# Optimization experiments

Measured on AMD Instinct MI355X. Metric: run time of the kernel, lower is better.

## Reference

```python
import jax, jax.numpy as jnp
import numpy as np

B, T, C, H, W = 1, 8, 64, 96, 96
DG = 16  # deform groups
MAX_RES = 5.0  # max_residue_magnitude


def lrelu(x):
    return jnp.where(x >= 0, x, 0.1 * x)


def conv(x, w, b):
    y = jax.lax.conv_general_dilated(x, w, (1, 1), 'SAME',
                                     dimension_numbers=('NCHW', 'OIHW', 'NCHW'))
    return y + b[None, :, None, None]


def mod_deform_conv2d(x, offset, mask, weight, bias, dg):
    # Modulated deformable conv v2: 3x3 kernel, stride 1, pad 1, dil 1.
    Bs, Cin, Hs, Ws = x.shape
    K = 9
    cpg = Cin // dg
    Cout = weight.shape[0]
    off = offset.reshape(Bs, dg, K, 2, Hs, Ws)  # (y, x) per tap
    m = mask.reshape(Bs, dg, K, Hs, Ws)
    ky = jnp.repeat(jnp.arange(3), 3).astype(x.dtype)
    kx = jnp.tile(jnp.arange(3), 3).astype(x.dtype)
    # base sampling positions: out_pos - pad + tap*dil
    py = (jnp.arange(Hs, dtype=x.dtype) - 1.0)[None, :, None] + ky[:, None, None]  # (K,H,1)
    px = (jnp.arange(Ws, dtype=x.dtype) - 1.0)[None, None, :] + kx[:, None, None]  # (K,1,W)
    sy = off[:, :, :, 0] + py  # (B,dg,K,H,W)
    sx = off[:, :, :, 1] + px
    y0 = jnp.floor(sy)
    x0 = jnp.floor(sx)
    fy = sy - y0
    fx = sx - x0
    y0i = y0.astype(jnp.int32)
    x0i = x0.astype(jnp.int32)
    xf = x.reshape(Bs, dg, cpg, Hs * Ws)

    def gather(yi, xi, wgt):
        valid = (yi >= 0) & (yi < Hs) & (xi >= 0) & (xi < Ws)
        idx = (jnp.clip(yi, 0, Hs - 1) * Ws + jnp.clip(xi, 0, Ws - 1))
        idx = idx.reshape(Bs, dg, 1, K * Hs * Ws)
        v = jnp.take_along_axis(xf, idx, axis=3).reshape(Bs, dg, cpg, K, Hs, Ws)
        return v * (wgt * valid)[:, :, None]

    val = (gather(y0i, x0i, (1 - fy) * (1 - fx))
           + gather(y0i, x0i + 1, (1 - fy) * fx)
           + gather(y0i + 1, x0i, fy * (1 - fx))
           + gather(y0i + 1, x0i + 1, fy * fx))
    cols = val * m[:, :, None]  # (B,dg,cpg,K,H,W)
    wr = weight.reshape(Cout, dg, cpg, K)
    out = jnp.einsum('ogck,bgckhw->bohw', wr, cols)
    return out + bias[None, :, None, None]


def deform_align(xin, cond, p):
    h = lrelu(conv(cond, p['ow1'], p['ob1']))
    h = lrelu(conv(h, p['ow2'], p['ob2']))
    h = lrelu(conv(h, p['ow3'], p['ob3']))
    out = conv(h, p['ow4'], p['ob4'])
    offset = MAX_RES * jnp.tanh(out[:, :18 * DG])
    mask = jax.nn.sigmoid(out[:, 18 * DG:])
    return mod_deform_conv2d(xin, offset, mask, p['dw'], p['db'], DG)


def bidir_prop(x, params):
    t = x.shape[1]
    spatial = [x[:, i] for i in range(t)]
    feats = {}
    for name, rev in (('backward_', True), ('forward_', False)):
        p = params[name]
        order = list(range(t))[::-1] if rev else list(range(t))
        out_list = []
        prop = jnp.zeros_like(spatial[0])
        for i, idx in enumerate(order):
            cur = spatial[idx]
            if i > 0:
                feat_n2 = out_list[-2] if i > 1 else jnp.zeros_like(prop)
                cond = jnp.concatenate([prop, cur, feat_n2], axis=1)
                prop = deform_align(jnp.concatenate([prop, feat_n2], axis=1), cond, p)
            if name == 'forward_':
                feat = jnp.concatenate([cur, feats['backward_'][idx], prop], axis=1)
            else:
                feat = jnp.concatenate([cur, prop], axis=1)
            prop = prop + conv(lrelu(conv(feat, p['bw1'], p['bb1'])), p['bw2'], p['bb2'])
            out_list.append(prop)
        feats[name] = out_list[::-1] if rev else out_list
    fw, fb = params['fusion']
    outs = [conv(jnp.concatenate([feats['backward_'][i], feats['forward_'][i]], axis=1), fw, fb)
            for i in range(t)]
    return jnp.stack(outs, axis=1) + x


def setup_inputs() -> dict:
    key = jax.random.key(0)
    ks = iter(jax.random.split(key, 64))

    def w(*shape):
        return jax.random.normal(next(ks), shape, jnp.float32) * 0.03

    def b(n):
        return jnp.zeros((n,), jnp.float32)

    d = {'x': jax.random.normal(next(ks), (B, T, C, H, W), jnp.float32)}
    for pre, bb1_in in (('b', 2 * C), ('f', 3 * C)):
        d[pre + '_dw'] = w(C, 2 * C, 3, 3); d[pre + '_db'] = b(C)
        d[pre + '_ow1'] = w(C, 3 * C, 3, 3); d[pre + '_ob1'] = b(C)
        d[pre + '_ow2'] = w(C, C, 3, 3); d[pre + '_ob2'] = b(C)
        d[pre + '_ow3'] = w(C, C, 3, 3); d[pre + '_ob3'] = b(C)
        d[pre + '_ow4'] = w(27 * DG, C, 3, 3); d[pre + '_ob4'] = b(27 * DG)
        d[pre + '_bw1'] = w(C, bb1_in, 3, 3); d[pre + '_bb1'] = b(C)
        d[pre + '_bw2'] = w(C, C, 3, 3); d[pre + '_bb2'] = b(C)
    d['fus_w'] = w(C, 2 * C, 1, 1)
    d['fus_b'] = b(C)
    return d


def _assemble(b_dw, b_db, b_ow1, b_ob1, b_ow2, b_ob2, b_ow3, b_ob3, b_ow4, b_ob4,
              b_bw1, b_bb1, b_bw2, b_bb2,
              f_dw, f_db, f_ow1, f_ob1, f_ow2, f_ob2, f_ow3, f_ob3, f_ow4, f_ob4,
              f_bw1, f_bb1, f_bw2, f_bb2, fus_w, fus_b):
    return {
        'backward_': dict(dw=b_dw, db=b_db, ow1=b_ow1, ob1=b_ob1, ow2=b_ow2, ob2=b_ob2,
                          ow3=b_ow3, ob3=b_ob3, ow4=b_ow4, ob4=b_ob4,
                          bw1=b_bw1, bb1=b_bb1, bw2=b_bw2, bb2=b_bb2),
        'forward_': dict(dw=f_dw, db=f_db, ow1=f_ow1, ob1=f_ob1, ow2=f_ow2, ob2=f_ob2,
                         ow3=f_ow3, ob3=f_ob3, ow4=f_ow4, ob4=f_ob4,
                         bw1=f_bw1, bb1=f_bb1, bw2=f_bw2, bb2=f_bb2),
        'fusion': (fus_w, fus_b),
    }


def reference(x, b_dw, b_db, b_ow1, b_ob1, b_ow2, b_ob2, b_ow3, b_ob3, b_ow4, b_ob4,
              b_bw1, b_bb1, b_bw2, b_bb2,
              f_dw, f_db, f_ow1, f_ob1, f_ow2, f_ob2, f_ow3, f_ob3, f_ow4, f_ob4,
              f_bw1, f_bb1, f_bw2, f_bb2, fus_w, fus_b):
    params = _assemble(b_dw, b_db, b_ow1, b_ob1, b_ow2, b_ob2, b_ow3, b_ob3, b_ow4, b_ob4,
                       b_bw1, b_bb1, b_bw2, b_bb2,
                       f_dw, f_db, f_ow1, f_ob1, f_ow2, f_ob2, f_ow3, f_ob3, f_ow4, f_ob4,
                       f_bw1, f_bb1, f_bw2, f_bb2, fus_w, fus_b)
    return bidir_prop(x, params)
```

## Files before the change

### kernel.cpp

```cpp
#include <hip/hip_runtime.h>
#include <cstddef>
#include <cstdint>

#define HW96 9216
#define FRAME (64 * 9216)

typedef unsigned short ushort_t;
typedef __attribute__((ext_vector_type(8))) short bf16x8;
typedef __attribute__((ext_vector_type(4))) float f32x4;
typedef __attribute__((ext_vector_type(4))) unsigned u32x4;
typedef __attribute__((ext_vector_type(8))) ushort_t u16x8;
typedef __attribute__((ext_vector_type(4))) ushort_t u16x4;

__device__ __forceinline__ float unpk(unsigned p) {
    return __uint_as_float(p & 0xFFFF0000u) + __uint_as_float(p << 16);
}
__device__ __forceinline__ unsigned pk(float v) {
    unsigned u = __float_as_uint(v);
    unsigned hi = u & 0xFFFF0000u;
    float rem = v - __uint_as_float(hi);
    unsigned r = __float_as_uint(rem);
    unsigned lo = (r + 0x7FFFu + ((r >> 16) & 1u)) >> 16;
    return hi | (lo & 0xFFFFu);
}
__device__ __forceinline__ void split16(float v, ushort_t& h, ushort_t& l) {
    unsigned u = __float_as_uint(v);
    h = (ushort_t)(u >> 16);
    float rem = v - __uint_as_float(u & 0xFFFF0000u);
    unsigned r = __float_as_uint(rem);
    l = (ushort_t)((r + 0x7FFFu + ((r >> 16) & 1u)) >> 16);
}
__device__ __forceinline__ ushort_t bf16rnd(float v) {
    unsigned u = __float_as_uint(v);
    return (ushort_t)((u + 0x7FFFu + ((u >> 16) & 1u)) >> 16);
}
__device__ __forceinline__ float bfh(ushort_t h) {
    return __uint_as_float(((unsigned)h) << 16);
}

struct FragJob { const float* src; ushort_t* dst; int O, I, OT, KC, mode; };
struct FragJobs { FragJob j[15]; };

__global__ __launch_bounds__(256) void frag_all_k(FragJobs jobs) {
    const FragJob& J = jobs.j[blockIdx.y];
    int idx = blockIdx.x * 256 + threadIdx.x;
    int total = ((J.mode == 0) ? 9 : 1) * J.KC * J.OT * 512;
    if (idx >= total) return;
    int jj = idx & 7;
    int lane = (idx >> 3) & 63;
    int rem = idx >> 9;
    int ot = rem % J.OT;
    rem /= J.OT;
    int cc = rem % J.KC;
    int t = rem / J.KC;
    int o = ot * 16 + (lane & 15);
    float wv = 0.f;
    if (J.mode == 0) {
        int ci = cc * 32 + (lane >> 4) * 8 + jj;
        if (o < J.O && ci < J.I) wv = J.src[(o * J.I + ci) * 9 + t];
    } else if (J.mode == 1) {
        int K = cc * 32 + (lane >> 4) * 8 + jj;
        int g = K / 72, r2 = K % 72;
        int tap = r2 >> 3, c = r2 & 7;
        int ci = g * 8 + c;
        if (o < J.O && ci < J.I) wv = J.src[(o * J.I + ci) * 9 + tap];
    } else {
        int ci = cc * 32 + (lane >> 4) * 8 + jj;
        if (o < J.O && ci < J.I) wv = J.src[o * J.I + ci];
    }
    ushort_t h, l;
    split16(wv, h, l);
    J.dst[idx] = h;
    J.dst[total + idx] = l;
}

__global__ __launch_bounds__(256) void pack_tr_k(const float* __restrict__ src,
                                                 unsigned* __restrict__ dst,
                                                 ushort_t* __restrict__ dsth) {
    const int t = blockIdx.y;
    const int px0 = blockIdx.x * 64;
    __shared__ unsigned tile[64 * 65];
    const float* s = src + (size_t)t * FRAME;
    unsigned* d = dst + (size_t)t * FRAME;
    ushort_t* dh = dsth + (size_t)t * FRAME;
#pragma unroll
    for (int it = 0; it < 16; ++it) {
        int e = it * 256 + threadIdx.x;
        int p = e & 63, ch = e >> 6;
        tile[ch * 65 + p] = pk(s[(size_t)ch * HW96 + px0 + p]);
    }
    __syncthreads();
#pragma unroll
    for (int it = 0; it < 16; ++it) {
        int e = it * 256 + threadIdx.x;
        int ch = e & 63, p = e >> 6;
        unsigned v = tile[ch * 65 + p];
        d[(size_t)(px0 + p) * 64 + ch] = v;
        dh[(size_t)(px0 + p) * 64 + ch] = (ushort_t)(v >> 16);
    }
}

template <int TERMS>
__global__ __launch_bounds__(128, 3) void convm_k(
    const unsigned* __restrict__ s0, const unsigned* __restrict__ s1,
    const unsigned* __restrict__ s2, int b0, int b1, int b2, int nsrc,
    const ushort_t* __restrict__ wfrag, int KCfull,
    const float* __restrict__ bias, const float* __restrict__ addsrc,
    const float* __restrict__ addsrc2, const float* __restrict__ abias,
    ushort_t* __restrict__ outhi, unsigned* __restrict__ outpk, int act) {
    const int tid = threadIdx.x;
    const int lane = tid & 63;
    const int w = tid >> 6;
    const int h = blockIdx.x & 1;
    const int bseg = blockIdx.x >> 1;
    const int ot = h * 2 + w;
    const int xb = (bseg % 6) * 16;
    const int y = bseg / 6;
    const int n = lane & 15;
    const int quad = lane >> 4;

    __shared__ __align__(16) ushort_t ldsH[3 * 18 * 72];
    __shared__ __align__(16) ushort_t ldsL[3 * 18 * 72];

    int jst[4], jok[4], joff[4], jbase[4];
#pragma unroll
    for (int i = 0; i < 4; ++i) {
        int e = tid + i * 128;
        int rc = e >> 3, cg = e & 7;
        int r = rc / 18, col = rc - r * 18;
        int gy = y - 1 + r, gx = xb - 1 + col;
        jst[i] = (e < 432);
        jok[i] = jst[i] && ((unsigned)gy < 96u) && ((unsigned)gx < 96u);
        joff[i] = (gy * 96 + gx) * 64 + cg * 8;
        jbase[i] = rc * 72 + cg * 8;
    }

    f32x4 acc0, acc1;
#pragma unroll
    for (int r = 0; r < 4; ++r) { acc0[r] = 0.f; acc1[r] = 0.f; }

    const size_t hlOff = (size_t)9 * KCfull * 4 * 512;

    for (int j = 0; j < nsrc; ++j) {
        const unsigned* sv = (j == 0) ? s0 : (j == 1 ? s1 : s2);
        const int base = (j == 0) ? b0 : (j == 1 ? b1 : b2);
        __syncthreads();
#pragma unroll
        for (int i = 0; i < 4; ++i) {
            if (jst[i]) {
                u32x4 a, b;
                if (jok[i]) {
                    a = *(const u32x4*)(sv + joff[i]);
                    b = *(const u32x4*)(sv + joff[i] + 4);
                } else {
#pragma unroll
                    for (int q = 0; q < 4; ++q) { a[q] = 0; b[q] = 0; }
                }
                u32x4 H, L;
#pragma unroll
                for (int q = 0; q < 2; ++q) {
                    H[q] = (a[2 * q] >> 16) | (a[2 * q + 1] & 0xFFFF0000u);
                    L[q] = (a[2 * q] & 0xFFFFu) | (a[2 * q + 1] << 16);
                    H[2 + q] = (b[2 * q] >> 16) | (b[2 * q + 1] & 0xFFFF0000u);
                    L[2 + q] = (b[2 * q] & 0xFFFFu) | (b[2 * q + 1] << 16);
                }
                *(u32x4*)(ldsH + jbase[i]) = H;
                *(u32x4*)(ldsL + jbase[i]) = L;
            }
        }
        __syncthreads();
        bf16x8 pAh[5], pAl[5], pBh[5], pBl[5];
#pragma unroll
        for (int s = 0; s < 23; ++s) {
            if (s >= 5) {
                const int u = s - 5;
                const bf16x8 Ah = pAh[u % 5];
                const bf16x8 Bh = pBh[u % 5], Bl = pBl[u % 5];
                if (u & 1) {
                    acc1 = __builtin_amdgcn_mfma_f32_16x16x32_bf16(Ah, Bh, acc1, 0, 0, 0);
                    if (TERMS == 3)
                        acc1 = __builtin_amdgcn_mfma_f32_16x16x32_bf16(pAl[u % 5], Bh, acc1, 0, 0, 0);
                    acc1 = __builtin_amdgcn_mfma_f32_16x16x32_bf16(Ah, Bl, acc1, 0, 0, 0);
                } else {
                    acc0 = __builtin_amdgcn_mfma_f32_16x16x32_bf16(Ah, Bh, acc0, 0, 0, 0);
                    if (TERMS == 3)
                        acc0 = __builtin_amdgcn_mfma_f32_16x16x32_bf16(pAl[u % 5], Bh, acc0, 0, 0, 0);
                    acc0 = __builtin_amdgcn_mfma_f32_16x16x32_bf16(Ah, Bl, acc0, 0, 0, 0);
                }
            }
            if (s < 18) {
                const int t = s >> 1, cc2 = s & 1;
                const int ky = t / 3, kx = t % 3;
                const int ccor = base + cc2;
                const ushort_t* ab =
                    wfrag + (((size_t)(t * KCfull + ccor) * 4 + ot) * 64 + lane) * 8;
                pAh[s % 5] = *(const bf16x8*)ab;
                if (TERMS == 3) pAl[s % 5] = *(const bf16x8*)(ab + hlOff);
                const int lb = (ky * 18 + n + kx) * 72 + cc2 * 32 + quad * 8;
                pBh[s % 5] = *(const bf16x8*)(ldsH + lb);
                pBl[s % 5] = *(const bf16x8*)(ldsL + lb);
            }
        }
    }

    const int px = y * 96 + xb + n;
    u16x4 hi4;
#pragma unroll
    for (int r = 0; r < 4; ++r) {
        int cout = ot * 16 + quad * 4 + r;
        float v = acc0[r] + acc1[r] + bias[cout];
        if (act) v = (v >= 0.f) ? v : 0.1f * v;
        if (addsrc) {
            size_t off = (size_t)cout * HW96 + px;
            v += addsrc[off] + addsrc2[off] + abias[cout];
        }
        outpk[(size_t)px * 64 + cout] = pk(v);
        hi4[r] = bf16rnd(v);
    }
    if (outhi)
        *(u16x4*)(outhi + (size_t)px * 64 + ot * 16 + quad * 4) = hi4;
}

__global__ __launch_bounds__(128, 3) void convh_k(
    const ushort_t* __restrict__ s0, const ushort_t* __restrict__ s1,
    const ushort_t* __restrict__ s2, int b0, int b1, int b2, int nsrc,
    const ushort_t* __restrict__ wfrag, int KCfull,
    const float* __restrict__ bias, ushort_t* __restrict__ outhi, int act) {
    const int tid = threadIdx.x;
    const int lane = tid & 63;
    const int w = tid >> 6;
    const int h = blockIdx.x & 1;
    const int bseg = blockIdx.x >> 1;
    const int ot = h * 2 + w;
    const int xb = (bseg % 6) * 16;
    const int y = bseg / 6;
    const int n = lane & 15;
    const int quad = lane >> 4;

    __shared__ __align__(16) ushort_t ldsH[3 * 18 * 72];

    int jst[4], jok[4], joff[4], jbase[4];
#pragma unroll
    for (int i = 0; i < 4; ++i) {
        int e = tid + i * 128;
        int rc = e >> 3, cg = e & 7;
        int r = rc / 18, col = rc - r * 18;
        int gy = y - 1 + r, gx = xb - 1 + col;
        jst[i] = (e < 432);
        jok[i] = jst[i] && ((unsigned)gy < 96u) && ((unsigned)gx < 96u);
        joff[i] = (gy * 96 + gx) * 64 + cg * 8;
        jbase[i] = rc * 72 + cg * 8;
    }

    f32x4 acc0, acc1;
#pragma unroll
    for (int r = 0; r < 4; ++r) { acc0[r] = 0.f; acc1[r] = 0.f; }

    for (int j = 0; j < nsrc; ++j) {
        const ushort_t* sv = (j == 0) ? s0 : (j == 1 ? s1 : s2);
        const int base = (j == 0) ? b0 : (j == 1 ? b1 : b2);
        __syncthreads();
#pragma unroll
        for (int i = 0; i < 4; ++i) {
            if (jst[i]) {
                u16x8 a;
                if (jok[i]) {
                    a = *(const u16x8*)(sv + joff[i]);
                } else {
#pragma unroll
                    for (int q = 0; q < 8; ++q) a[q] = 0;
                }
                *(u16x8*)(ldsH + jbase[i]) = a;
            }
        }
        __syncthreads();
        bf16x8 pAh[5], pBh[5];
#pragma unroll
        for (int s = 0; s < 23; ++s) {
            if (s >= 5) {
                const int u = s - 5;
                const bf16x8 Ah = pAh[u % 5];
                const bf16x8 Bh = pBh[u % 5];
                if (u & 1)
                    acc1 = __builtin_amdgcn_mfma_f32_16x16x32_bf16(Ah, Bh, acc1, 0, 0, 0);
                else
                    acc0 = __builtin_amdgcn_mfma_f32_16x16x32_bf16(Ah, Bh, acc0, 0, 0, 0);
            }
            if (s < 18) {
                const int t = s >> 1, cc2 = s & 1;
                const int ky = t / 3, kx = t % 3;
                const int ccor = base + cc2;
                const ushort_t* ab =
                    wfrag + (((size_t)(t * KCfull + ccor) * 4 + ot) * 64 + lane) * 8;
                pAh[s % 5] = *(const bf16x8*)ab;
                const int lb = (ky * 18 + n + kx) * 72 + cc2 * 32 + quad * 8;
                pBh[s % 5] = *(const bf16x8*)(ldsH + lb);
            }
        }
    }

    const int px = y * 96 + xb + n;
    u16x4 hi4;
#pragma unroll
    for (int r = 0; r < 4; ++r) {
        int cout = ot * 16 + quad * 4 + r;
        float v = acc0[r] + acc1[r] + bias[cout];
        if (act) v = (v >= 0.f) ? v : 0.1f * v;
        hi4[r] = bf16rnd(v);
    }
    *(u16x4*)(outhi + (size_t)px * 64 + ot * 16 + quad * 4) = hi4;
}

__global__ __launch_bounds__(256) void dconv_fused_k(
    const ushort_t* __restrict__ sAh, const ushort_t* __restrict__ sBh,
    const ushort_t* __restrict__ hAh, const ushort_t* __restrict__ w4,
    const float* __restrict__ ob4, const ushort_t* __restrict__ dwf,
    int ngr4, float* __restrict__ pacc) {
    const int tid = threadIdx.x;
    const int lane = tid & 63;
    const int w = tid >> 6;
    const int h = blockIdx.x & 1;
    const int seg = blockIdx.x >> 1;
    const int xb = (seg % 6) * 16;
    const int y = seg / 6;
    const int n = lane & 15;
    const int quad = lane >> 4;

    __shared__ __align__(16) char smem[15232 + 18944];
    float* rawS = (float*)smem;
    ushort_t* ldsAH = (ushort_t*)(smem + 15232);
    ushort_t* colsH = (ushort_t*)(smem + 15232);
    ushort_t* colsL = colsH + 4736;

    const int nrounds = ngr4 >> 1;
    const int ng = nrounds * 4;
    const int g0 = h * ng;
    const int otO_s = (g0 * 18) >> 4;
    const int otO_e = (g0 * 18 + ng * 18 - 1) >> 4;
    const int nO = otO_e - otO_s + 1;
    const int otM_s = (288 + g0 * 9) >> 4;
    const int otM_e = (288 + g0 * 9 + ng * 9 - 1) >> 4;
    const int nM = otM_e - otM_s + 1;
    const int nt = nO + nM;
    const int rowOffO = otO_s * 16;
    const int rowOffM = otM_s * 16 - nO * 16;

#pragma unroll
    for (int i = 0; i < 2; ++i) {
        int e = tid + i * 256;
        if (e < 432) {
            int rc = e >> 3, cg = e & 7;
            int r = rc / 18, col = rc - r * 18;
            int gy = y - 1 + r, gx = xb - 1 + col;
            bool ok = ((unsigned)gy < 96u) && ((unsigned)gx < 96u);
            u16x8 a;
            if (ok) {
                a = *(const u16x8*)(hAh + (gy * 96 + gx) * 64 + cg * 8);
            } else {
#pragma unroll
                for (int q = 0; q < 8; ++q) a[q] = 0;
            }
            *(u16x8*)(ldsAH + rc * 72 + cg * 8) = a;
        }
    }
    __syncthreads();

#pragma unroll 1
    for (int j = 0; j < 4; ++j) {
        const int idx = j * 4 + w;
        if (idx >= nt) break;
        const int ot = (idx < nO) ? (otO_s + idx) : (otM_s + (idx - nO));
        f32x4 a0, a1;
#pragma unroll
        for (int r = 0; r < 4; ++r) { a0[r] = 0.f; a1[r] = 0.f; }
        bf16x8 pAh[5], pBh[5];
#pragma unroll
        for (int s = 0; s < 23; ++s) {
            if (s >= 5) {
                const int u = s - 5;
                const bf16x8 Ah = pAh[u % 5];
                const bf16x8 Bh = pBh[u % 5];
                if (u & 1)
                    a1 = __builtin_amdgcn_mfma_f32_16x16x32_bf16(Ah, Bh, a1, 0, 0, 0);
                else
                    a0 = __builtin_amdgcn_mfma_f32_16x16x32_bf16(Ah, Bh, a0, 0, 0, 0);
            }
            if (s < 18) {
                const int t = s >> 1, cc2 = s & 1;
                const int ky = t / 3, kx = t % 3;
                const ushort_t* ab =
                    w4 + (((size_t)s * 28 + ot) * 64 + lane) * 8;
                pAh[s % 5] = *(const bf16x8*)ab;
                const int lb = (ky * 18 + n + kx) * 72 + cc2 * 32 + quad * 8;
                pBh[s % 5] = *(const bf16x8*)(ldsAH + lb);
            }
        }
#pragma unroll
        for (int r = 0; r < 4; ++r) {
            int cout = ot * 16 + quad * 4 + r;
            float v = a0[r] + a1[r] + (cout < 432 ? ob4[cout] : 0.f);
            rawS[(idx * 16 + quad * 4 + r) * 17 + n] = v;
        }
    }

    f32x4 acc0, acc1;
#pragma unroll
    for (int r = 0; r < 4; ++r) { acc0[r] = 0.f; acc1[r] = 0.f; }

    for (int gci = 0; gci < nrounds; ++gci) {
        const int gc = h * nrounds + gci;
        __syncthreads();
#pragma unroll
        for (int i = 0; i < 3; ++i) {
            int e = tid + i * 256;
            if (e < 576) {
                int p = e & 15;
                int r = e >> 4;
                int gl = r / 9, k = r - gl * 9;
                int g = gc * 4 + gl;
                float ry = rawS[(g * 18 + k * 2 + 0 - rowOffO) * 17 + p];
                float rx = rawS[(g * 18 + k * 2 + 1 - rowOffO) * 17 + p];
                float rm = rawS[(288 + g * 9 + k - rowOffM) * 17 + p];
                float oy = 5.f * (1.f - 2.f / (1.f + __expf(2.f * ry)));
                float ox = 5.f * (1.f - 2.f / (1.f + __expf(2.f * rx)));
                float m = 1.f / (1.f + __expf(-rm));
                float sy = oy + (float)(y - 1 + k / 3);
                float sx = ox + (float)(xb + p - 1 + k % 3);
                float fy0 = floorf(sy), fx0 = floorf(sx);
                float fy = sy - fy0, fx = sx - fx0;
                int y0 = (int)fy0, x0 = (int)fx0;
                int y1 = y0 + 1, x1 = x0 + 1;
                bool vy0 = (unsigned)y0 < 96u, vy1 = (unsigned)y1 < 96u;
                bool vx0 = (unsigned)x0 < 96u, vx1 = (unsigned)x1 < 96u;
                int cy0 = min(max(y0, 0), 95), cy1 = min(max(y1, 0), 95);
                int cx0 = min(max(x0, 0), 95), cx1 = min(max(x1, 0), 95);
                float w00 = (1.f - fy) * (1.f - fx) * ((vy0 && vx0) ? 1.f : 0.f);
                float w01 = (1.f - fy) * fx * ((vy0 && vx1) ? 1.f : 0.f);
                float w10 = fy * (1.f - fx) * ((vy1 && vx0) ? 1.f : 0.f);
                float w11 = fy * fx * ((vy1 && vx1) ? 1.f : 0.f);
                const ushort_t* src = (g < 8) ? sAh : sBh;
                int cb = (g & 7) * 8;
                int kbase = p * 296 + gl * 72 + k * 8;
                ushort_t hh[8], ll[8];
                if (src) {
                    u16x8 c00 = *(const u16x8*)(src + (cy0 * 96 + cx0) * 64 + cb);
                    u16x8 c01 = *(const u16x8*)(src + (cy0 * 96 + cx1) * 64 + cb);
                    u16x8 c10 = *(const u16x8*)(src + (cy1 * 96 + cx0) * 64 + cb);
                    u16x8 c11 = *(const u16x8*)(src + (cy1 * 96 + cx1) * 64 + cb);
#pragma unroll
                    for (int c = 0; c < 8; ++c) {
                        float v = w00 * bfh(c00[c]) + w01 * bfh(c01[c]) +
                                  w10 * bfh(c10[c]) + w11 * bfh(c11[c]);
                        split16(v * m, hh[c], ll[c]);
                    }
                } else {
#pragma unroll
                    for (int c = 0; c < 8; ++c) { hh[c] = 0; ll[c] = 0; }
                }
                u32x4 H, L;
#pragma unroll
                for (int q = 0; q < 4; ++q) {
                    H[q] = (unsigned)hh[2 * q] | ((unsigned)hh[2 * q + 1] << 16);
                    L[q] = (unsigned)ll[2 * q] | ((unsigned)ll[2 * q + 1] << 16);
                }
                *(u32x4*)(colsH + kbase) = H;
                *(u32x4*)(colsL + kbase) = L;
            }
        }
        __syncthreads();
        bf16x8 qAh[4], qBh[4], qBl[4];
#pragma unroll
        for (int s = 0; s < 13; ++s) {
            if (s >= 4) {
                const int u = s - 4;
                const bf16x8 Ah = qAh[u % 4];
                const bf16x8 Bh = qBh[u % 4], Bl = qBl[u % 4];
                if (u & 1) {
                    acc1 = __builtin_amdgcn_mfma_f32_16x16x32_bf16(Ah, Bh, acc1, 0, 0, 0);
                    acc1 = __builtin_amdgcn_mfma_f32_16x16x32_bf16(Ah, Bl, acc1, 0, 0, 0);
                } else {
                    acc0 = __builtin_amdgcn_mfma_f32_16x16x32_bf16(Ah, Bh, acc0, 0, 0, 0);
                    acc0 = __builtin_amdgcn_mfma_f32_16x16x32_bf16(Ah, Bl, acc0, 0, 0, 0);
                }
            }
            if (s < 9) {
                const int cc = gc * 9 + s;
                const ushort_t* ab = dwf + (((size_t)cc * 4 + w) * 64 + lane) * 8;
                qAh[s % 4] = *(const bf16x8*)ab;
                const int lb = n * 296 + s * 32 + quad * 8;
                qBh[s % 4] = *(const bf16x8*)(colsH + lb);
                qBl[s % 4] = *(const bf16x8*)(colsL + lb);
            }
        }
    }

    const int pidx = y * 96 + xb + n;
#pragma unroll
    for (int r = 0; r < 4; ++r) {
        int cout = w * 16 + quad * 4 + r;
        pacc[(size_t)h * FRAME + (size_t)cout * HW96 + pidx] =
            acc0[r] + acc1[r];
    }
}

__global__ __launch_bounds__(256) void dcomb_k(const float* __restrict__ pacc,
                                               const float* __restrict__ dbias,
                                               unsigned* __restrict__ outpk) {
    const int px0 = blockIdx.x * 64;
    __shared__ unsigned tile[64 * 65];
#pragma unroll
    for (int it = 0; it < 16; ++it) {
        int e = it * 256 + threadIdx.x;
        int p = e & 63, ch = e >> 6;
        size_t off = (size_t)ch * HW96 + px0 + p;
        float v = pacc[off] + pacc[(size_t)FRAME + off] + dbias[ch];
        tile[ch * 65 + p] = pk(v);
    }
    __syncthreads();
#pragma unroll
    for (int it = 0; it < 16; ++it) {
        int e = it * 256 + threadIdx.x;
        int ch = e & 63, p = e >> 6;
        outpk[(size_t)(px0 + p) * 64 + ch] = tile[ch * 65 + p];
    }
}

__global__ __launch_bounds__(128) void fusem_k(
    const unsigned* __restrict__ featB, const unsigned* __restrict__ featF,
    const float* __restrict__ x, const ushort_t* __restrict__ wfrag,
    const float* __restrict__ bias, float* __restrict__ out) {
    const int tid = threadIdx.x;
    const int lane = tid & 63;
    const int w = tid >> 6;
    const int h = blockIdx.x & 1;
    const int bseg = blockIdx.x >> 1;
    const int t = blockIdx.y;
    const int ot = h * 2 + w;
    const int xb = (bseg % 6) * 16;
    const int y = bseg / 6;
    const int n = lane & 15;
    const int quad = lane >> 4;

    __shared__ __align__(16) ushort_t ldsH[16 * 144];
    __shared__ __align__(16) ushort_t ldsL[16 * 144];

    const int p = tid >> 3, cg = tid & 7;
    const int off = ((y * 96 + xb + p) * 64 + cg * 8);
#pragma unroll
    for (int i = 0; i < 2; ++i) {
        const unsigned* sv =
            (i == 0 ? featB : featF) + (size_t)t * FRAME;
        u32x4 a = *(const u32x4*)(sv + off);
        u32x4 b = *(const u32x4*)(sv + off + 4);
        u32x4 H, L;
#pragma unroll
        for (int q = 0; q < 2; ++q) {
            H[q] = (a[2 * q] >> 16) | (a[2 * q + 1] & 0xFFFF0000u);
            L[q] = (a[2 * q] & 0xFFFFu) | (a[2 * q + 1] << 16);
            H[2 + q] = (b[2 * q] >> 16) | (b[2 * q + 1] & 0xFFFF0000u);
            L[2 + q] = (b[2 * q] & 0xFFFFu) | (b[2 * q + 1] << 16);
        }
        *(u32x4*)(ldsH + p * 144 + i * 64 + cg * 8) = H;
        *(u32x4*)(ldsL + p * 144 + i * 64 + cg * 8) = L;
    }
    __syncthreads();

    f32x4 acc0, acc1;
#pragma unroll
    for (int r = 0; r < 4; ++r) { acc0[r] = 0.f; acc1[r] = 0.f; }
    const size_t hlOff = (size_t)4 * 4 * 512;
#pragma unroll
    for (int cc = 0; cc < 4; ++cc) {
        const ushort_t* ab = wfrag + (((size_t)cc * 4 + ot) * 64 + lane) * 8;
        bf16x8 Ah = *(const bf16x8*)ab;
        bf16x8 Al = *(const bf16x8*)(ab + hlOff);
        int lb = n * 144 + cc * 32 + quad * 8;
        bf16x8 Bh = *(const bf16x8*)(ldsH + lb);
        bf16x8 Bl = *(const bf16x8*)(ldsL + lb);
        if (cc & 1) {
            acc1 = __builtin_amdgcn_mfma_f32_16x16x32_bf16(Ah, Bh, acc1, 0, 0, 0);
            acc1 = __builtin_amdgcn_mfma_f32_16x16x32_bf16(Al, Bh, acc1, 0, 0, 0);
            acc1 = __builtin_amdgcn_mfma_f32_16x16x32_bf16(Ah, Bl, acc1, 0, 0, 0);
        } else {
            acc0 = __builtin_amdgcn_mfma_f32_16x16x32_bf16(Ah, Bh, acc0, 0, 0, 0);
            acc0 = __builtin_amdgcn_mfma_f32_16x16x32_bf16(Al, Bh, acc0, 0, 0, 0);
            acc0 = __builtin_amdgcn_mfma_f32_16x16x32_bf16(Ah, Bl, acc0, 0, 0, 0);
        }
    }

    const int pidx = y * 96 + xb + n;
    const float* xt = x + (size_t)t * FRAME;
    float* od = out + (size_t)t * FRAME;
#pragma unroll
    for (int r = 0; r < 4; ++r) {
        int cout = ot * 16 + quad * 4 + r;
        size_t o2 = (size_t)cout * HW96 + pidx;
        od[o2] = acc0[r] + acc1[r] + bias[cout] + xt[o2];
    }
}

extern "C" void kernel_launch(void* const* d_in, const int* in_sizes, int n_in,
                              void* d_out, int out_size, void* d_ws,
                              size_t ws_size, hipStream_t stream) {
    const float* x = (const float*)d_in[0];
    auto gp = [&](int i) { return (const float*)d_in[i]; };

    struct DirP {
        const float *dw, *db, *ow1, *ob1, *ow2, *ob2, *ow3, *ob3, *ow4, *ob4,
            *bw1, *bb1, *bw2, *bb2;
    };
    DirP Pb{gp(1), gp(2), gp(3), gp(4), gp(5), gp(6), gp(7),
            gp(8), gp(9), gp(10), gp(11), gp(12), gp(13), gp(14)};
    DirP Pf{gp(15), gp(16), gp(17), gp(18), gp(19), gp(20), gp(21),
            gp(22), gp(23), gp(24), gp(25), gp(26), gp(27), gp(28)};
    const float* fus_w = gp(29);
    const float* fus_b = gp(30);

    unsigned* featBpk = (unsigned*)d_ws;
    unsigned* featFpk = featBpk + (size_t)8 * FRAME;
    unsigned* xpk = featFpk + (size_t)8 * FRAME;
    unsigned* Dpk = xpk + (size_t)8 * FRAME;
    unsigned* hApk = Dpk + FRAME;
    unsigned* hBpk = hApk + FRAME;
    ushort_t* fragp = (ushort_t*)(hBpk + FRAME);

    auto falloc = [&](size_t nelem) {
        ushort_t* p = fragp;
        fragp += nelem;
        return p;
    };

    struct DirW { ushort_t *ow1, *ow2, *ow3, *ow4, *bw1, *bw2, *dw; int bw1KC; };
    FragJobs fj;
    int nf = 0;
    auto fjob = [&](const float* src, int O, int I, int OT, int KC) {
        ushort_t* dst = falloc((size_t)2 * 9 * KC * OT * 512);
        fj.j[nf++] = FragJob{src, dst, O, I, OT, KC, 0};
        return dst;
    };
    auto fjobd = [&](const float* src) {
        ushort_t* dst = falloc((size_t)2 * 36 * 4 * 512);
        fj.j[nf++] = FragJob{src, dst, 64, 128, 4, 36, 1};
        return dst;
    };
    DirW Wb, Wf;
    Wb.ow1 = fjob(Pb.ow1, 64, 192, 4, 6);
    Wb.ow2 = fjob(Pb.ow2, 64, 64, 4, 2);
    Wb.ow3 = fjob(Pb.ow3, 64, 64, 4, 2);
    Wb.ow4 = fjob(Pb.ow4, 432, 64, 28, 2);
    Wb.bw1 = fjob(Pb.bw1, 64, 128, 4, 4);
    Wb.bw1KC = 4;
    Wb.bw2 = fjob(Pb.bw2, 64, 64, 4, 2);
    Wb.dw = fjobd(Pb.dw);
    Wf.ow1 = fjob(Pf.ow1, 64, 192, 4, 6);
    Wf.ow2 = fjob(Pf.ow2, 64, 64, 4, 2);
    Wf.ow3 = fjob(Pf.ow3, 64, 64, 4, 2);
    Wf.ow4 = fjob(Pf.ow4, 432, 64, 28, 2);
    Wf.bw1 = fjob(Pf.bw1, 64, 192, 4, 6);
    Wf.bw1KC = 6;
    Wf.bw2 = fjob(Pf.bw2, 64, 64, 4, 2);
    Wf.dw = fjobd(Pf.dw);
    ushort_t* Wfus = falloc((size_t)2 * 4 * 4 * 512);
    fj.j[nf++] = FragJob{fus_w, Wfus, 64, 128, 4, 4, 2};
    frag_all_k<<<dim3(1008, 15), 256, 0, stream>>>(fj);

    float* pacc = (float*)((((uintptr_t)fragp) + 15) & ~(uintptr_t)15);
    ushort_t* featBh = (ushort_t*)(pacc + (size_t)2 * FRAME);
    ushort_t* featFh = featBh + (size_t)8 * FRAME;
    ushort_t* xh = featFh + (size_t)8 * FRAME;
    ushort_t* hAh = (ushort_t*)hApk;
    ushort_t* hBh = (ushort_t*)hBpk;

    pack_tr_k<<<dim3(144, 8), 256, 0, stream>>>(x, xpk, xh);

    auto convm = [&](const unsigned* a, const unsigned* b, const unsigned* c2,
                     const ushort_t* frag, int KCfull, const float* bias,
                     const float* add, const float* add2, const float* abias,
                     ushort_t* outhi, unsigned* out, int act, int terms) {
        const unsigned* srcs[3] = {a, b, c2};
        const unsigned* S[3] = {nullptr, nullptr, nullptr};
        int B[3] = {0, 0, 0};
        int ns = 0;
        for (int j = 0; j < 3; ++j)
            if (srcs[j]) {
                S[ns] = srcs[j];
                B[ns] = j * 2;
                ++ns;
            }
        if (terms == 2)
            convm_k<2><<<1152, 128, 0, stream>>>(S[0], S[1], S[2], B[0], B[1],
                                                 B[2], ns, frag, KCfull, bias,
                                                 add, add2, abias, outhi, out,
                                                 act);
        else
            convm_k<3><<<1152, 128, 0, stream>>>(S[0], S[1], S[2], B[0], B[1],
                                                 B[2], ns, frag, KCfull, bias,
                                                 add, add2, abias, outhi, out,
                                                 act);
    };

    auto convh = [&](const ushort_t* a, const ushort_t* b, const ushort_t* c2,
                     const ushort_t* frag, int KCfull, const float* bias,
                     ushort_t* out, int act) {
        const ushort_t* srcs[3] = {a, b, c2};
        const ushort_t* S[3] = {nullptr, nullptr, nullptr};
        int B[3] = {0, 0, 0};
        int ns = 0;
        for (int j = 0; j < 3; ++j)
            if (srcs[j]) {
                S[ns] = srcs[j];
                B[ns] = j * 2;
                ++ns;
            }
        convh_k<<<1152, 128, 0, stream>>>(S[0], S[1], S[2], B[0], B[1], B[2],
                                          ns, frag, KCfull, bias, out, act);
    };

    for (int dir = 0; dir < 2; ++dir) {
        const DirP& P = dir ? Pf : Pb;
        const DirW& W = dir ? Wf : Wb;
        unsigned* feat = dir ? featFpk : featBpk;
        ushort_t* feath = dir ? featFh : featBh;
        const unsigned* prev1 = nullptr;
        const unsigned* prev2 = nullptr;
        const ushort_t* prev1h = nullptr;
        const ushort_t* prev2h = nullptr;
        for (int i = 0; i < 8; ++i) {
            int idx = dir ? i : 7 - i;
            const unsigned* cur = xpk + (size_t)idx * FRAME;
            const ushort_t* curh = xh + (size_t)idx * FRAME;
            bool hasD = false;
            if (i > 0) {
                convh(prev1h, curh, prev2h, W.ow1, 6, P.ob1, hAh, 1);
                convh(hAh, nullptr, nullptr, W.ow2, 2, P.ob2, hBh, 1);
                convh(hBh, nullptr, nullptr, W.ow3, 2, P.ob3, hAh, 1);
                int ngr4 = (prev2 != nullptr) ? 4 : 2;
                dconv_fused_k<<<1152, 256, 0, stream>>>(
                    prev1h, prev2h, hAh, W.ow4, P.ob4, W.dw, ngr4, pacc);
                dcomb_k<<<144, 256, 0, stream>>>(pacc, P.db, Dpk);
                hasD = true;
            }
            unsigned* dst = feat + (size_t)idx * FRAME;
            ushort_t* dsth = feath + (size_t)idx * FRAME;
            if (dir == 0) {
                convm(cur, hasD ? Dpk : nullptr, nullptr, W.bw1, W.bw1KC,
                      P.bb1, nullptr, nullptr, nullptr, nullptr, hBpk, 1, 2);
            } else {
                convm(cur, featBpk + (size_t)idx * FRAME,
                      hasD ? Dpk : nullptr, W.bw1, W.bw1KC, P.bb1, nullptr,
                      nullptr, nullptr, nullptr, hBpk, 1, 2);
            }
            convm(hBpk, nullptr, nullptr, W.bw2, 2, P.bb2,
                  hasD ? pacc : nullptr, pacc + FRAME, P.db, dsth, dst, 0, 3);
            prev2 = prev1;
            prev1 = dst;
            prev2h = prev1h;
            prev1h = dsth;
        }
    }

    fusem_k<<<dim3(1152, 8), 128, 0, stream>>>(featBpk, featFpk, x, Wfus,
                                               fus_b, (float*)d_out);
}
```

Measured before the change: 1.303 ms.

## Fuse deform-conv partial combine into consumer conv and switch pacc to pixel-major

Removes the separate dcomb_k kernel by having convm_k read the two fp32 partial sums plus bias directly while staging its LDS tile, splitting them into hi/lo bf16 on the fly. The partial-sum buffer is changed from channel-major to pixel-major so both the staging loads and the residual-add epilogue use contiguous vector loads. The second convm also drops from 3-term to 2-term split precision, cutting one MFMA per step at some accuracy risk.

```diff
diff --git a/kernel.cpp b/kernel.cpp
--- a/kernel.cpp
+++ b/kernel.cpp
@@ -103,11 +103,12 @@
 template <int TERMS>
 __global__ __launch_bounds__(128, 3) void convm_k(
     const unsigned* __restrict__ s0, const unsigned* __restrict__ s1,
-    const unsigned* __restrict__ s2, int b0, int b1, int b2, int nsrc,
-    const ushort_t* __restrict__ wfrag, int KCfull,
-    const float* __restrict__ bias, const float* __restrict__ addsrc,
-    const float* __restrict__ addsrc2, const float* __restrict__ abias,
-    ushort_t* __restrict__ outhi, unsigned* __restrict__ outpk, int act) {
+    int nsrc, int dslot, const float* __restrict__ dpacc,
+    const float* __restrict__ ddbias, const ushort_t* __restrict__ wfrag,
+    int KCfull, const float* __restrict__ bias,
+    const float* __restrict__ addsrc, const float* __restrict__ addsrc2,
+    const float* __restrict__ abias, ushort_t* __restrict__ outhi,
+    unsigned* __restrict__ outpk, int act) {
     const int tid = threadIdx.x;
     const int lane = tid & 63;
     const int w = tid >> 6;
@@ -142,30 +143,64 @@
     const size_t hlOff = (size_t)9 * KCfull * 4 * 512;
 
     for (int j = 0; j < nsrc; ++j) {
-        const unsigned* sv = (j == 0) ? s0 : (j == 1 ? s1 : s2);
-        const int base = (j == 0) ? b0 : (j == 1 ? b1 : b2);
+        const int base = j * 2;
         __syncthreads();
-#pragma unroll
-        for (int i = 0; i < 4; ++i) {
-            if (jst[i]) {
-                u32x4 a, b;
-                if (jok[i]) {
-                    a = *(const u32x4*)(sv + joff[i]);
-                    b = *(const u32x4*)(sv + joff[i] + 4);
-                } else {
-#pragma unroll
-                    for (int q = 0; q < 4; ++q) { a[q] = 0; b[q] = 0; }
+        if (j == dslot) {
+#pragma unroll
+            for (int i = 0; i < 4; ++i) {
+                if (jst[i]) {
+                    ushort_t hh[8], ll[8];
+                    if (jok[i]) {
+                        const int cg8 = ((tid + i * 128) & 7) << 3;
+                        f32x4 a0 = *(const f32x4*)(dpacc + joff[i]);
+                        f32x4 a1 = *(const f32x4*)(dpacc + joff[i] + 4);
+                        f32x4 b0 = *(const f32x4*)(dpacc + FRAME + joff[i]);
+                        f32x4 b1 = *(const f32x4*)(dpacc + FRAME + joff[i] + 4);
+                        f32x4 d0 = *(const f32x4*)(ddbias + cg8);
+                        f32x4 d1 = *(const f32x4*)(ddbias + cg8 + 4);
+#pragma unroll
+                        for (int q = 0; q < 4; ++q) {
+                            split16(a0[q] + b0[q] + d0[q], hh[q], ll[q]);
+                            split16(a1[q] + b1[q] + d1[q], hh[4 + q], ll[4 + q]);
+                        }
+                    } else {
+#pragma unroll
+                        for (int q = 0; q < 8; ++q) { hh[q] = 0; ll[q] = 0; }
+                    }
+                    u32x4 H, L;
+#pragma unroll
+                    for (int q = 0; q < 4; ++q) {
+                        H[q] = (unsigned)hh[2 * q] | ((unsigned)hh[2 * q + 1] << 16);
+                        L[q] = (unsigned)ll[2 * q] | ((unsigned)ll[2 * q + 1] << 16);
+                    }
+                    *(u32x4*)(ldsH + jbase[i]) = H;
+                    *(u32x4*)(ldsL + jbase[i]) = L;
                 }
-                u32x4 H, L;
-#pragma unroll
-                for (int q = 0; q < 2; ++q) {
-                    H[q] = (a[2 * q] >> 16) | (a[2 * q + 1] & 0xFFFF0000u);
-                    L[q] = (a[2 * q] & 0xFFFFu) | (a[2 * q + 1] << 16);
-                    H[2 + q] = (b[2 * q] >> 16) | (b[2 * q + 1] & 0xFFFF0000u);
-                    L[2 + q] = (b[2 * q] & 0xFFFFu) | (b[2 * q + 1] << 16);
+            }
+        } else {
+            const unsigned* sv = (j == 0) ? s0 : s1;
+#pragma unroll
+            for (int i = 0; i < 4; ++i) {
+                if (jst[i]) {
+                    u32x4 a, b;
+                    if (jok[i]) {
+                        a = *(const u32x4*)(sv + joff[i]);
+                        b = *(const u32x4*)(sv + joff[i] + 4);
+                    } else {
+#pragma unroll
+                        for (int q = 0; q < 4; ++q) { a[q] = 0; b[q] = 0; }
+                    }
+                    u32x4 H, L;
+#pragma unroll
+                    for (int q = 0; q < 2; ++q) {
+                        H[q] = (a[2 * q] >> 16) | (a[2 * q + 1] & 0xFFFF0000u);
+                        L[q] = (a[2 * q] & 0xFFFFu) | (a[2 * q + 1] << 16);
+                        H[2 + q] = (b[2 * q] >> 16) | (b[2 * q + 1] & 0xFFFF0000u);
+                        L[2 + q] = (b[2 * q] & 0xFFFFu) | (b[2 * q + 1] << 16);
+                    }
+                    *(u32x4*)(ldsH + jbase[i]) = H;
+                    *(u32x4*)(ldsL + jbase[i]) = L;
                 }
-                *(u32x4*)(ldsH + jbase[i]) = H;
-                *(u32x4*)(ldsL + jbase[i]) = L;
             }
         }
         __syncthreads();
@@ -204,16 +239,20 @@
     }
 
     const int px = y * 96 + xb + n;
+    f32x4 pa, pb;
+#pragma unroll
+    for (int r = 0; r < 4; ++r) { pa[r] = 0.f; pb[r] = 0.f; }
+    if (addsrc) {
+        pa = *(const f32x4*)(addsrc + (size_t)px * 64 + ot * 16 + quad * 4);
+        pb = *(const f32x4*)(addsrc2 + (size_t)px * 64 + ot * 16 + quad * 4);
+    }
     u16x4 hi4;
 #pragma unroll
     for (int r = 0; r < 4; ++r) {
         int cout = ot * 16 + quad * 4 + r;
         float v = acc0[r] + acc1[r] + bias[cout];
         if (act) v = (v >= 0.f) ? v : 0.1f * v;
-        if (addsrc) {
-            size_t off = (size_t)cout * HW96 + px;
-            v += addsrc[off] + addsrc2[off] + abias[cout];
-        }
+        if (addsrc) v += pa[r] + pb[r] + abias[cout];
         outpk[(size_t)px * 64 + cout] = pk(v);
         hi4[r] = bf16rnd(v);
     }
@@ -495,34 +534,11 @@
     }
 
     const int pidx = y * 96 + xb + n;
-#pragma unroll
-    for (int r = 0; r < 4; ++r) {
-        int cout = w * 16 + quad * 4 + r;
-        pacc[(size_t)h * FRAME + (size_t)cout * HW96 + pidx] =
-            acc0[r] + acc1[r];
-    }
-}
-
-__global__ __launch_bounds__(256) void dcomb_k(const float* __restrict__ pacc,
-                                               const float* __restrict__ dbias,
-                                               unsigned* __restrict__ outpk) {
-    const int px0 = blockIdx.x * 64;
-    __shared__ unsigned tile[64 * 65];
-#pragma unroll
-    for (int it = 0; it < 16; ++it) {
-        int e = it * 256 + threadIdx.x;
-        int p = e & 63, ch = e >> 6;
-        size_t off = (size_t)ch * HW96 + px0 + p;
-        float v = pacc[off] + pacc[(size_t)FRAME + off] + dbias[ch];
-        tile[ch * 65 + p] = pk(v);
-    }
-    __syncthreads();
-#pragma unroll
-    for (int it = 0; it < 16; ++it) {
-        int e = it * 256 + threadIdx.x;
-        int ch = e & 63, p = e >> 6;
-        outpk[(size_t)(px0 + p) * 64 + ch] = tile[ch * 65 + p];
-    }
+    f32x4 sv;
+#pragma unroll
+    for (int r = 0; r < 4; ++r) sv[r] = acc0[r] + acc1[r];
+    *(f32x4*)(pacc + (size_t)h * FRAME + (size_t)pidx * 64 + w * 16 +
+              quad * 4) = sv;
 }
 
 __global__ __launch_bounds__(128) void fusem_k(
@@ -619,8 +635,7 @@
     unsigned* featBpk = (unsigned*)d_ws;
     unsigned* featFpk = featBpk + (size_t)8 * FRAME;
     unsigned* xpk = featFpk + (size_t)8 * FRAME;
-    unsigned* Dpk = xpk + (size_t)8 * FRAME;
-    unsigned* hApk = Dpk + FRAME;
+    unsigned* hApk = xpk + (size_t)8 * FRAME;
     unsigned* hBpk = hApk + FRAME;
     ushort_t* fragp = (ushort_t*)(hBpk + FRAME);
 
@@ -673,30 +688,25 @@
 
     pack_tr_k<<<dim3(144, 8), 256, 0, stream>>>(x, xpk, xh);
 
-    auto convm = [&](const unsigned* a, const unsigned* b, const unsigned* c2,
-                     const ushort_t* frag, int KCfull, const float* bias,
-                     const float* add, const float* add2, const float* abias,
-                     ushort_t* outhi, unsigned* out, int act, int terms) {
-        const unsigned* srcs[3] = {a, b, c2};
-        const unsigned* S[3] = {nullptr, nullptr, nullptr};
-        int B[3] = {0, 0, 0};
+    auto convm = [&](const unsigned* a, const unsigned* b, int withD,
+                     const float* ddbias, const ushort_t* frag, int KCfull,
+                     const float* bias, const float* add, const float* add2,
+                     const float* abias, ushort_t* outhi, unsigned* out,
+                     int act, int terms) {
+        const unsigned* S[2] = {nullptr, nullptr};
         int ns = 0;
-        for (int j = 0; j < 3; ++j)
-            if (srcs[j]) {
-                S[ns] = srcs[j];
-                B[ns] = j * 2;
-                ++ns;
-            }
+        if (a) S[ns++] = a;
+        if (b) S[ns++] = b;
+        int dslot = -1;
+        if (withD) { dslot = ns; ++ns; }
         if (terms == 2)
-            convm_k<2><<<1152, 128, 0, stream>>>(S[0], S[1], S[2], B[0], B[1],
-                                                 B[2], ns, frag, KCfull, bias,
-                                                 add, add2, abias, outhi, out,
-                                                 act);
+            convm_k<2><<<1152, 128, 0, stream>>>(
+                S[0], S[1], ns, dslot, pacc, ddbias, frag, KCfull, bias, add,
+                add2, abias, outhi, out, act);
         else
-            convm_k<3><<<1152, 128, 0, stream>>>(S[0], S[1], S[2], B[0], B[1],
-                                                 B[2], ns, frag, KCfull, bias,
-                                                 add, add2, abias, outhi, out,
-                                                 act);
+            convm_k<3><<<1152, 128, 0, stream>>>(
+                S[0], S[1], ns, dslot, pacc, ddbias, frag, KCfull, bias, add,
+                add2, abias, outhi, out, act);
     };
 
     auto convh = [&](const ushort_t* a, const ushort_t* b, const ushort_t* c2,
@@ -722,7 +732,6 @@
         unsigned* feat = dir ? featFpk : featBpk;
         ushort_t* feath = dir ? featFh : featBh;
         const unsigned* prev1 = nullptr;
-        const unsigned* prev2 = nullptr;
         const ushort_t* prev1h = nullptr;
         const ushort_t* prev2h = nullptr;
         for (int i = 0; i < 8; ++i) {
@@ -734,29 +743,28 @@
                 convh(prev1h, curh, prev2h, W.ow1, 6, P.ob1, hAh, 1);
                 convh(hAh, nullptr, nullptr, W.ow2, 2, P.ob2, hBh, 1);
                 convh(hBh, nullptr, nullptr, W.ow3, 2, P.ob3, hAh, 1);
-                int ngr4 = (prev2 != nullptr) ? 4 : 2;
+                int ngr4 = (prev2h != nullptr) ? 4 : 2;
                 dconv_fused_k<<<1152, 256, 0, stream>>>(
                     prev1h, prev2h, hAh, W.ow4, P.ob4, W.dw, ngr4, pacc);
-                dcomb_k<<<144, 256, 0, stream>>>(pacc, P.db, Dpk);
                 hasD = true;
             }
             unsigned* dst = feat + (size_t)idx * FRAME;
             ushort_t* dsth = feath + (size_t)idx * FRAME;
             if (dir == 0) {
-                convm(cur, hasD ? Dpk : nullptr, nullptr, W.bw1, W.bw1KC,
-                      P.bb1, nullptr, nullptr, nullptr, nullptr, hBpk, 1, 2);
+                convm(cur, nullptr, hasD ? 1 : 0, P.db, W.bw1, W.bw1KC, P.bb1,
+                      nullptr, nullptr, nullptr, nullptr, hBpk, 1, 2);
             } else {
-                convm(cur, featBpk + (size_t)idx * FRAME,
-                      hasD ? Dpk : nullptr, W.bw1, W.bw1KC, P.bb1, nullptr,
-                      nullptr, nullptr, nullptr, hBpk, 1, 2);
-            }
-            convm(hBpk, nullptr, nullptr, W.bw2, 2, P.bb2,
-                  hasD ? pacc : nullptr, pacc + FRAME, P.db, dsth, dst, 0, 3);
-            prev2 = prev1;
+                convm(cur, featBpk + (size_t)idx * FRAME, hasD ? 1 : 0, P.db,
+                      W.bw1, W.bw1KC, P.bb1, nullptr, nullptr, nullptr,
+                      nullptr, hBpk, 1, 2);
+            }
+            convm(hBpk, nullptr, 0, nullptr, W.bw2, 2, P.bb2,
+                  hasD ? pacc : nullptr, pacc + FRAME, P.db, dsth, dst, 0, 2);
             prev1 = dst;
             prev2h = prev1h;
             prev1h = dsth;
         }
+        (void)prev1;
     }
 
     fusem_k<<<dim3(1152, 8), 128, 0, stream>>>(featBpk, featFpk, x, Wfus,
```

Result: faster. 1.240 ms (-4.8%).
